# Kernel tuning notes

Measured on AMD Instinct MI355X. Metric: run time of the kernel, lower is better.

The kernel has to match this reference:

```python
import jax, jax.numpy as jnp
import numpy as np

B, IN_DIM, HID = 8192, 1024, 1024

def setup_inputs() -> dict:
    key = jax.random.key(0)
    ks = jax.random.split(key, 11)
    s_in = 1.0 / np.sqrt(IN_DIM + HID)  # torch Linear default init scale
    inp = {
        "Z": jax.random.normal(ks[0], (B, IN_DIM), dtype=jnp.float32),
        "h_prev": jax.random.normal(ks[1], (B, HID), dtype=jnp.float32),
        "c_prev": jax.random.normal(ks[2], (B, HID), dtype=jnp.float32),
        "W_i": jax.random.uniform(ks[3], (IN_DIM + HID, HID), jnp.float32, -s_in, s_in),
        "b_i": jax.random.uniform(ks[4], (HID,), jnp.float32, -s_in, s_in),
        "W_f": jax.random.uniform(ks[5], (IN_DIM + HID, HID), jnp.float32, -s_in, s_in),
        "b_f": jax.random.uniform(ks[6], (HID,), jnp.float32, -s_in, s_in),
        "W_o": jax.random.uniform(ks[7], (IN_DIM + HID, HID), jnp.float32, -s_in, s_in),
        "b_o": jax.random.uniform(ks[8], (HID,), jnp.float32, -s_in, s_in),
        "W_g": jax.random.uniform(ks[9], (IN_DIM + HID, HID), jnp.float32, -s_in, s_in),
        "b_g": jax.random.uniform(ks[10], (HID,), jnp.float32, -s_in, s_in),
    }
    return inp

def reference(Z, h_prev, c_prev, W_i, b_i, W_f, b_f, W_o, b_o, W_g, b_g):
    combined = jnp.concatenate([Z, h_prev], axis=1)  # [B, IN+HID]
    i = jax.nn.sigmoid(combined @ W_i + b_i)
    f = jax.nn.sigmoid(combined @ W_f + b_f)
    o = jax.nn.sigmoid(combined @ W_o + b_o)
    g = jnp.tanh(combined @ W_g + b_g)
    c = f * c_prev + i * g
    h = o * jnp.tanh(c)
    return (h, c)
```

## Files before the change

kernel.cpp:

```cpp
#include <hip/hip_runtime.h>


#define BDIM 8192
#define KDIM 2048
#define NDIM 1024
#define NCAT 4096

typedef __bf16 bf16x8 __attribute__((ext_vector_type(8)));
typedef __bf16 bf16x4 __attribute__((ext_vector_type(4)));
typedef float  f32x4  __attribute__((ext_vector_type(4)));

__device__ __forceinline__ void async_cp16(const void* g, void* l) {
    __builtin_amdgcn_global_load_lds((__attribute__((address_space(1))) void*)g,
                                     (__attribute__((address_space(3))) void*)l,
                                     16, 0, 0);
}

__device__ __forceinline__ float sigm(float x) { return 1.f / (1.f + __expf(-x)); }
__device__ __forceinline__ float tanh_fast(float x) { return 1.f - 2.f / (1.f + __expf(2.f * x)); }

__global__ void prep_kernel(const float* __restrict__ Z, const float* __restrict__ H,
                            const float* __restrict__ Wi, const float* __restrict__ Wf,
                            const float* __restrict__ Wo, const float* __restrict__ Wg,
                            __bf16* __restrict__ A, __bf16* __restrict__ Wt) {
    __shared__ float t[32][33];
    int bid = blockIdx.x;
    if (bid < 16384) {
        int idx = bid * 256 + threadIdx.x;
        int row = idx >> 9;
        int q   = idx & 511;
        float4 v;
        if (q < 256) v = ((const float4*)Z)[row * 256 + q];
        else         v = ((const float4*)H)[row * 256 + (q - 256)];
        bf16x4 o = { (__bf16)v.x, (__bf16)v.y, (__bf16)v.z, (__bf16)v.w };
        ((bf16x4*)A)[idx] = o;
    } else {
        int id  = bid - 16384;
        int g   = id >> 11;
        int rem = id & 2047;
        int k0  = (rem & 63) * 32;
        int n0  = (rem >> 6) * 32;
        const float* W = (g == 0) ? Wi : (g == 1) ? Wf : (g == 2) ? Wo : Wg;
        int c = threadIdx.x & 31, r8 = threadIdx.x >> 5;
        #pragma unroll
        for (int j = 0; j < 4; ++j) {
            int r = r8 + j * 8;
            t[r][c] = W[(size_t)(k0 + r) * NDIM + (n0 + c)];
        }
        __syncthreads();
        size_t outRow = (size_t)((n0 >> 5) * 128 + g * 32);
        #pragma unroll
        for (int j = 0; j < 4; ++j) {
            int r = r8 + j * 8;
            Wt[(outRow + r) * KDIM + (k0 + c)] = (__bf16)t[c][r];
        }
    }
}

__global__ __launch_bounds__(256, 4)
void lstm_gemm_kernel(const __bf16* __restrict__ A, const __bf16* __restrict__ Wt,
                      const float* __restrict__ b_i, const float* __restrict__ b_f,
                      const float* __restrict__ b_o, const float* __restrict__ b_g,
                      const float* __restrict__ c_prev, float* __restrict__ out) {
    __shared__ char smem[32768];
    __bf16* As = (__bf16*)smem;
    __bf16* Bs = (__bf16*)(smem + 16384);
    float*  Ep = (float*)smem;

    const int tid  = threadIdx.x;
    const int wave = tid >> 6;
    const int lane = tid & 63;
    const int wr = wave >> 1, wc = wave & 1;

    const int bid = blockIdx.x;
    const int bx = (bid & 7) * 4 + ((bid >> 3) & 3);
    const int by = bid >> 5;
    const int m0 = by * 128;
    const int ncat0 = bx * 128;

    const int srow   = lane >> 2;
    const int schunk = (lane & 3) ^ ((lane >> 3) & 3);
    const __bf16* Ag[2]; __bf16* Al[2];
    const __bf16* Bg[2]; __bf16* Bl[2];
    #pragma unroll
    for (int i = 0; i < 2; ++i) {
        int grp = wave * 2 + i;
        Ag[i] = A  + (size_t)(m0    + grp * 16 + srow) * KDIM + schunk * 8;
        Bg[i] = Wt + (size_t)(ncat0 + grp * 16 + srow) * KDIM + schunk * 8;
        Al[i] = As + grp * 512;
        Bl[i] = Bs + grp * 512;
    }

    const int l15  = lane & 15;
    const int quad = lane >> 4;
    const int ksw  = (quad ^ ((l15 >> 1) & 3)) * 8;
    int aoff[4], boff[4];
    #pragma unroll
    for (int t = 0; t < 4; ++t) {
        aoff[t] = (wr * 64 + t * 16 + l15) * 32 + ksw;
        boff[t] = (wc * 64 + t * 16 + l15) * 32 + ksw;
    }

    f32x4 acc[4][4];
    #pragma unroll
    for (int i = 0; i < 4; ++i)
        #pragma unroll
        for (int j = 0; j < 4; ++j) acc[i][j] = (f32x4){0.f, 0.f, 0.f, 0.f};

    for (int k0 = 0; k0 < KDIM; k0 += 64) {
        #pragma unroll
        for (int h = 0; h < 2; ++h)
            #pragma unroll
            for (int i = 0; i < 2; ++i) {
                async_cp16(Ag[i] + k0 + h * 32, Al[i] + h * 4096);
                async_cp16(Bg[i] + k0 + h * 32, Bl[i] + h * 4096);
            }
        __syncthreads();

        #pragma unroll
        for (int h = 0; h < 2; ++h) {
            bf16x8 af[4], bfr[4];
            #pragma unroll
            for (int t = 0; t < 4; ++t) af[t]  = *(const bf16x8*)(As + h * 4096 + aoff[t]);
            #pragma unroll
            for (int t = 0; t < 4; ++t) bfr[t] = *(const bf16x8*)(Bs + h * 4096 + boff[t]);
            #pragma unroll
            for (int mt = 0; mt < 4; ++mt)
                #pragma unroll
                for (int nt = 0; nt < 4; ++nt)
                    acc[mt][nt] = __builtin_amdgcn_mfma_f32_16x16x32_bf16(af[mt], bfr[nt], acc[mt][nt], 0, 0, 0);
        }
        __syncthreads();
    }

    const float* bias_lo = (wc == 0) ? b_i : b_o;
    const float* bias_hi = (wc == 0) ? b_f : b_g;
    float bv[4];
    bv[0] = bias_lo[bx * 32 + l15];
    bv[1] = bias_lo[bx * 32 + 16 + l15];
    bv[2] = bias_hi[bx * 32 + l15];
    bv[3] = bias_hi[bx * 32 + 16 + l15];

    #pragma unroll
    for (int c = 0; c < 4; ++c) {
        __syncthreads();
        if (wr == (c >> 1)) {
            #pragma unroll
            for (int mi = 0; mi < 2; ++mi) {
                int mt = (c & 1) * 2 + mi;
                #pragma unroll
                for (int nt = 0; nt < 4; ++nt)
                    #pragma unroll
                    for (int r = 0; r < 4; ++r)
                        Ep[(mi * 16 + quad * 4 + r) * 132 + wc * 64 + nt * 16 + l15] =
                            acc[mt][nt][r] + bv[nt];
            }
        }
        __syncthreads();

        #pragma unroll
        for (int e = 0; e < 4; ++e) {
            int idx = tid + e * 256;
            int row = idx >> 5, n = idx & 31;
            float gi = sigm(Ep[row * 132 + n]);
            float gf = sigm(Ep[row * 132 + 32 + n]);
            float go = sigm(Ep[row * 132 + 64 + n]);
            float gg = tanh_fast(Ep[row * 132 + 96 + n]);
            size_t pos = (size_t)(m0 + c * 32 + row) * NDIM + bx * 32 + n;
            float cp = c_prev[pos];
            float cv = gf * cp + gi * gg;
            out[pos] = go * tanh_fast(cv);
            out[(size_t)BDIM * NDIM + pos] = cv;
        }
    }
}

extern "C" void kernel_launch(void* const* d_in, const int* in_sizes, int n_in,
                              void* d_out, int out_size, void* d_ws, size_t ws_size,
                              hipStream_t stream) {
    const float* Z  = (const float*)d_in[0];
    const float* H  = (const float*)d_in[1];
    const float* Cp = (const float*)d_in[2];
    const float* Wi = (const float*)d_in[3];
    const float* bi = (const float*)d_in[4];
    const float* Wf = (const float*)d_in[5];
    const float* bf = (const float*)d_in[6];
    const float* Wo = (const float*)d_in[7];
    const float* bo = (const float*)d_in[8];
    const float* Wg = (const float*)d_in[9];
    const float* bg = (const float*)d_in[10];

    __bf16* Acomb = (__bf16*)d_ws;
    __bf16* Wt    = (__bf16*)((char*)d_ws + (size_t)33554432);

    prep_kernel<<<16384 + 8192, 256, 0, stream>>>(Z, H, Wi, Wf, Wo, Wg, Acomb, Wt);
    lstm_gemm_kernel<<<dim3(NCAT / 128 * BDIM / 128), 256, 0, stream>>>(
        Acomb, Wt, bi, bf, bo, bg, Cp, (float*)d_out);
}
```

Baseline: 331.8 us.

## Interleave gate weight rows so LSTM epilogue runs from registers without LDS

The weight concat layout is reordered so each wave's 16-column MFMA tiles hold the i,f,o,g gates for the same hidden columns. The epilogue can then apply the gate math straight from accumulators, with nontemporal loads and stores, and no LDS staging or barriers. The prep kernel now converts 8 floats per thread, and the GEMM grid moves to a plain 2D launch, dropping the swizzled block order. Stores are now 16-lane rows rather than fully coalesced 32-wide rows, and L2 locality from the old block swizzle is lost.

New measurement: 359.5 us. +8.3%, slower.

```diff
diff --git a/kernel.cpp b/kernel.cpp
--- a/kernel.cpp
+++ b/kernel.cpp
@@ -25,17 +25,19 @@
                             __bf16* __restrict__ A, __bf16* __restrict__ Wt) {
     __shared__ float t[32][33];
     int bid = blockIdx.x;
-    if (bid < 16384) {
+    if (bid < 8192) {
         int idx = bid * 256 + threadIdx.x;
-        int row = idx >> 9;
-        int q   = idx & 511;
-        float4 v;
-        if (q < 256) v = ((const float4*)Z)[row * 256 + q];
-        else         v = ((const float4*)H)[row * 256 + (q - 256)];
-        bf16x4 o = { (__bf16)v.x, (__bf16)v.y, (__bf16)v.z, (__bf16)v.w };
-        ((bf16x4*)A)[idx] = o;
+        int row = idx >> 8;
+        int q   = idx & 255;
+        const float* src = (q < 128) ? (Z + (size_t)row * 1024 + q * 8)
+                                     : (H + (size_t)row * 1024 + (q - 128) * 8);
+        float4 v0 = ((const float4*)src)[0];
+        float4 v1 = ((const float4*)src)[1];
+        bf16x8 o = { (__bf16)v0.x, (__bf16)v0.y, (__bf16)v0.z, (__bf16)v0.w,
+                     (__bf16)v1.x, (__bf16)v1.y, (__bf16)v1.z, (__bf16)v1.w };
+        ((bf16x8*)A)[idx] = o;
     } else {
-        int id  = bid - 16384;
+        int id  = bid - 8192;
         int g   = id >> 11;
         int rem = id & 2047;
         int k0  = (rem & 63) * 32;
@@ -48,11 +50,11 @@
             t[r][c] = W[(size_t)(k0 + r) * NDIM + (n0 + c)];
         }
         __syncthreads();
-        size_t outRow = (size_t)((n0 >> 5) * 128 + g * 32);
         #pragma unroll
         for (int j = 0; j < 4; ++j) {
             int r = r8 + j * 8;
-            Wt[(outRow + r) * KDIM + (k0 + c)] = (__bf16)t[c][r];
+            size_t catrow = (size_t)(n0 >> 5) * 128 + ((r >> 4) & 1) * 64 + g * 16 + (r & 15);
+            Wt[catrow * KDIM + (k0 + c)] = (__bf16)t[c][r];
         }
     }
 }
@@ -65,17 +67,13 @@
     __shared__ char smem[32768];
     __bf16* As = (__bf16*)smem;
     __bf16* Bs = (__bf16*)(smem + 16384);
-    float*  Ep = (float*)smem;
 
     const int tid  = threadIdx.x;
     const int wave = tid >> 6;
     const int lane = tid & 63;
     const int wr = wave >> 1, wc = wave & 1;
-
-    const int bid = blockIdx.x;
-    const int bx = (bid & 7) * 4 + ((bid >> 3) & 3);
-    const int by = bid >> 5;
-    const int m0 = by * 128;
+    const int bx = blockIdx.x;
+    const int m0 = blockIdx.y * 128;
     const int ncat0 = bx * 128;
 
     const int srow   = lane >> 2;
@@ -133,44 +131,28 @@
         __syncthreads();
     }
 
-    const float* bias_lo = (wc == 0) ? b_i : b_o;
-    const float* bias_hi = (wc == 0) ? b_f : b_g;
-    float bv[4];
-    bv[0] = bias_lo[bx * 32 + l15];
-    bv[1] = bias_lo[bx * 32 + 16 + l15];
-    bv[2] = bias_hi[bx * 32 + l15];
-    bv[3] = bias_hi[bx * 32 + 16 + l15];
+    const int col = bx * 32 + wc * 16 + l15;
+    const float b0 = b_i[col], b1 = b_f[col], b2 = b_o[col], b3 = b_g[col];
+    float* outC = out + (size_t)BDIM * NDIM;
 
     #pragma unroll
-    for (int c = 0; c < 4; ++c) {
-        __syncthreads();
-        if (wr == (c >> 1)) {
-            #pragma unroll
-            for (int mi = 0; mi < 2; ++mi) {
-                int mt = (c & 1) * 2 + mi;
-                #pragma unroll
-                for (int nt = 0; nt < 4; ++nt)
-                    #pragma unroll
-                    for (int r = 0; r < 4; ++r)
-                        Ep[(mi * 16 + quad * 4 + r) * 132 + wc * 64 + nt * 16 + l15] =
-                            acc[mt][nt][r] + bv[nt];
-            }
-        }
-        __syncthreads();
-
+    for (int mt = 0; mt < 4; ++mt) {
+        const size_t base = (size_t)(m0 + wr * 64 + mt * 16 + quad * 4) * NDIM + col;
+        float cp[4];
         #pragma unroll
-        for (int e = 0; e < 4; ++e) {
-            int idx = tid + e * 256;
-            int row = idx >> 5, n = idx & 31;
-            float gi = sigm(Ep[row * 132 + n]);
-            float gf = sigm(Ep[row * 132 + 32 + n]);
-            float go = sigm(Ep[row * 132 + 64 + n]);
-            float gg = tanh_fast(Ep[row * 132 + 96 + n]);
-            size_t pos = (size_t)(m0 + c * 32 + row) * NDIM + bx * 32 + n;
-            float cp = c_prev[pos];
-            float cv = gf * cp + gi * gg;
-            out[pos] = go * tanh_fast(cv);
-            out[(size_t)BDIM * NDIM + pos] = cv;
+        for (int r = 0; r < 4; ++r)
+            cp[r] = __builtin_nontemporal_load(c_prev + base + (size_t)r * NDIM);
+        #pragma unroll
+        for (int r = 0; r < 4; ++r) {
+            float gi = sigm(acc[mt][0][r] + b0);
+            float gf = sigm(acc[mt][1][r] + b1);
+            float go = sigm(acc[mt][2][r] + b2);
+            float gg = tanh_fast(acc[mt][3][r] + b3);
+            float cv = gf * cp[r] + gi * gg;
+            float hv = go * tanh_fast(cv);
+            size_t pos = base + (size_t)r * NDIM;
+            __builtin_nontemporal_store(hv, out + pos);
+            __builtin_nontemporal_store(cv, outC + pos);
         }
     }
 }
@@ -193,7 +175,7 @@
     __bf16* Acomb = (__bf16*)d_ws;
     __bf16* Wt    = (__bf16*)((char*)d_ws + (size_t)33554432);
 
-    prep_kernel<<<16384 + 8192, 256, 0, stream>>>(Z, H, Wi, Wf, Wo, Wg, Acomb, Wt);
-    lstm_gemm_kernel<<<dim3(NCAT / 128 * BDIM / 128), 256, 0, stream>>>(
+    prep_kernel<<<8192 + 8192, 256, 0, stream>>>(Z, H, Wi, Wf, Wo, Wg, Acomb, Wt);
+    lstm_gemm_kernel<<<dim3(NCAT / 128, BDIM / 128), 256, 0, stream>>>(
         Acomb, Wt, bi, bf, bo, bg, Cp, (float*)d_out);
 }
```
